# Kernel optimization log

Measured on AMD Instinct MI355X. Metric: run time of the kernel, lower is better.

The kernel has to match this reference:

```python
import jax, jax.numpy as jnp
import numpy as np

NN, D, H = 100000, 300, 1024   # nodes, embedding dim, hidden dim
NG, NS = 50000, 25000          # global vocab, sense vocab
B, T = 8, 128                  # batch, sequence length (state carried across all B*T steps)


def setup_inputs() -> dict:
    key = jax.random.key(0)
    ks = jax.random.split(key, 24)
    s = lambda i, shape: (jax.random.normal(ks[i], shape, jnp.float32) * 0.02)
    return {
        "x_idx": jax.random.randint(ks[0], (B, T), 0, NN),
        "X": jax.random.normal(ks[1], (NN, D), jnp.float32) * 0.1,
        "W_z_1": s(2, (D, H)), "U_z_1": s(3, (H, H)),
        "W_r_1": s(4, (D, H)), "U_r_1": s(5, (H, H)),
        "W_1": s(6, (D, H)), "b_W_1": jnp.zeros((H,), jnp.float32),
        "U_1": s(7, (H, H)), "b_U_1": jnp.zeros((H,), jnp.float32),
        "W_z_2": s(8, (H, H)), "U_z_2": s(9, (H, H)),
        "W_r_2": s(10, (H, H)), "U_r_2": s(11, (H, H)),
        "W_2": s(12, (H, H)), "b_W_2": jnp.zeros((H,), jnp.float32),
        "U_2": s(13, (H, H)), "b_U_2": jnp.zeros((H,), jnp.float32),
        "W_g": s(14, (H, NG)), "b_g": jnp.zeros((NG,), jnp.float32),
        "W_s": s(15, (H, NS)), "b_s": jnp.zeros((NS,), jnp.float32),
    }


def reference(x_idx, X, W_z_1, U_z_1, W_r_1, U_r_1, W_1, b_W_1, U_1, b_U_1,
              W_z_2, U_z_2, W_r_2, U_r_2, W_2, b_W_2, U_2, b_U_2,
              W_g, b_g, W_s, b_s):
    # The original loops over every sample of every sequence, carrying memory_h1/h2
    # across the whole batch; only X[x_indices[0]] feeds the GRU (the GAT-projected
    # neighbours are computed but never used). Dropout in eval mode = identity.
    idx = x_idx.reshape(-1)          # [S] flattened step order (seq-major per sample)
    emb = X[idx]                     # [S, D] currentword embeddings

    def step(carry, e):
        h1, h2 = carry
        z1 = jax.nn.sigmoid(e @ W_z_1 + h1 @ U_z_1)
        r1 = jax.nn.sigmoid(e @ W_r_1 + h1 @ U_r_1)
        ht1 = jnp.tanh((e @ W_1 + b_W_1) + ((r1 * h1) @ U_1 + b_U_1))
        h1n = z1 * ht1 + (1.0 - z1) * h1
        z2 = jax.nn.sigmoid(h1n @ W_z_2 + h2 @ U_z_2)
        r2 = jax.nn.sigmoid(h1n @ W_r_2 + h2 @ U_r_2)
        ht2 = jnp.tanh((h1n @ W_2 + b_W_2) + ((r2 * h2) @ U_2 + b_U_2))
        h2n = z2 * ht2 + (1.0 - z2) * h2
        return (h1n, h2n), h2n

    h0 = jnp.zeros((H,), emb.dtype)
    _, hs = jax.lax.scan(step, (h0, h0), emb)        # hs: [S, H]
    logp_g = jax.nn.log_softmax(hs @ W_g + b_g, axis=-1)   # [S, NG]
    logp_s = jax.nn.log_softmax(hs @ W_s + b_s, axis=-1)   # [S, NS]
    return logp_g, logp_s
```

## Files before the change

kernel.cpp:

```cpp
#include <hip/hip_runtime.h>

typedef __attribute__((ext_vector_type(4))) float f32x4;
typedef __attribute__((ext_vector_type(8))) __bf16 bf16x8;
typedef __attribute__((ext_vector_type(4))) unsigned short u16x4;

#define GPAD 40
#define KEEPF(x) asm volatile("" : "+v"(x))
#define PHYS(i) ((i) + (((i) >> 6) << 2))

__device__ unsigned long long g_h1s[1025 * 1024];
__device__ unsigned long long g_rh1[1024];
__device__ unsigned long long g_h2cur[1024];
__device__ unsigned long long g_rh2[1024];
__device__ float g_ExW[1024 * 3072];
__device__ float g_hs2[1024 * 1024];

__device__ __forceinline__ unsigned short f2bf(float x) {
  unsigned u = __builtin_bit_cast(unsigned, x);
  u += 0x7FFFu + ((u >> 16) & 1u);
  return (unsigned short)(u >> 16);
}
__device__ __forceinline__ unsigned long long packtv(unsigned tag, float v) {
  return ((unsigned long long)tag << 32) | (unsigned long long)__builtin_bit_cast(unsigned, v);
}
__device__ __forceinline__ unsigned long long aload(const unsigned long long* p) {
  return __hip_atomic_load(p, __ATOMIC_RELAXED, __HIP_MEMORY_SCOPE_AGENT);
}
__device__ __forceinline__ void astore(unsigned long long* p, unsigned long long v) {
  __hip_atomic_store(p, v, __ATOMIC_RELAXED, __HIP_MEMORY_SCOPE_AGENT);
}
__device__ __forceinline__ float lo32(unsigned long long v) {
  return __builtin_bit_cast(float, (unsigned)v);
}

__global__ void init_kernel() {
  int t = threadIdx.x;
  astore(&g_rh1[t], 0ull);
  astore(&g_h2cur[t], 0ull);
  astore(&g_rh2[t], 0ull);
}

__global__ __launch_bounds__(256, 1) void fused_scan(
    const float* __restrict__ ExW,
    const float* __restrict__ Uz1, const float* __restrict__ Ur1,
    const float* __restrict__ Uw1, const float* __restrict__ bU1,
    const float* __restrict__ Wz2, const float* __restrict__ Wr2,
    const float* __restrict__ Ww2,
    const float* __restrict__ Uz2, const float* __restrict__ Ur2,
    const float* __restrict__ Uw2,
    const float* __restrict__ bW2, const float* __restrict__ bU2,
    float* __restrict__ hs2)
{
  const int tid = threadIdx.x;
  const int c = tid & 15, q = tid >> 4;
  const int inw = tid & 63, wv = tid >> 6;
  __shared__ __align__(16) float h_s[1088];
  __shared__ __align__(16) float rh_s[1088];
  __shared__ __align__(16) float x_s[1088];
  __shared__ float pz[4][16], pr[4][16], pw[4][16];

  if (blockIdx.x < 64) {
    const int g = blockIdx.x;
    const int j = g * 16 + c;
    float uz[64], ur[64], uw[64];
#pragma unroll
    for (int i = 0; i < 64; ++i) uz[i] = Uz1[(size_t)(q * 64 + i) * 1024 + j];
#pragma unroll
    for (int i = 0; i < 64; ++i) ur[i] = Ur1[(size_t)(q * 64 + i) * 1024 + j];
#pragma unroll
    for (int i = 0; i < 64; ++i) uw[i] = Uw1[(size_t)(q * 64 + i) * 1024 + j];
#pragma unroll
    for (int i = 0; i < 64; ++i) { KEEPF(uz[i]); KEEPF(ur[i]); KEEPF(uw[i]); }
    const float bu = bU1[j];

    float zreg = 0.f, hold = 0.f;
    for (int s = 0; s < 1024; ++s) {
      float xz = 0.f, xr = 0.f, xw = 0.f;
      if (tid < 16) { xz = ExW[s * 3072 + j]; xw = ExW[s * 3072 + 2048 + j]; }
      else if (tid < 32) { xr = ExW[s * 3072 + 1024 + j]; }
      {
        const unsigned long long* sl = g_h1s + (size_t)s * 1024 + tid * 4;
        unsigned long long a0, a1, a2, a3;
        for (;;) {
          a0 = aload(sl); a1 = aload(sl + 1); a2 = aload(sl + 2); a3 = aload(sl + 3);
          unsigned bad = ((unsigned)(a0 >> 32) ^ (unsigned)s) | ((unsigned)(a1 >> 32) ^ (unsigned)s) |
                         ((unsigned)(a2 >> 32) ^ (unsigned)s) | ((unsigned)(a3 >> 32) ^ (unsigned)s);
          if (bad == 0u) break;
          __builtin_amdgcn_s_sleep(1);
        }
        f32x4 v; v.x = lo32(a0); v.y = lo32(a1); v.z = lo32(a2); v.w = lo32(a3);
        *(f32x4*)&h_s[PHYS(tid * 4)] = v;
      }
      __syncthreads();
      float az = 0.f, ar = 0.f;
      {
        const float* hp = h_s + q * 68;
#pragma unroll
        for (int i2 = 0; i2 < 16; ++i2) {
          f32x4 hv = *(const f32x4*)(hp + i2 * 4);
          az = fmaf(uz[i2 * 4 + 0], hv.x, az); az = fmaf(uz[i2 * 4 + 1], hv.y, az);
          az = fmaf(uz[i2 * 4 + 2], hv.z, az); az = fmaf(uz[i2 * 4 + 3], hv.w, az);
          ar = fmaf(ur[i2 * 4 + 0], hv.x, ar); ar = fmaf(ur[i2 * 4 + 1], hv.y, ar);
          ar = fmaf(ur[i2 * 4 + 2], hv.z, ar); ar = fmaf(ur[i2 * 4 + 3], hv.w, ar);
        }
      }
      az += __shfl_xor(az, 16, 64); az += __shfl_xor(az, 32, 64);
      ar += __shfl_xor(ar, 16, 64); ar += __shfl_xor(ar, 32, 64);
      if (inw < 16) { pz[wv][c] = az; pr[wv][c] = ar; }
      __syncthreads();
      if (tid < 32) {
        if (tid < 16) {
          float zz = pz[0][c] + pz[1][c] + pz[2][c] + pz[3][c] + xz;
          zreg = 1.f / (1.f + __expf(-zz));
          hold = h_s[PHYS(j)];
        } else {
          float rr = pr[0][c] + pr[1][c] + pr[2][c] + pr[3][c] + xr;
          float r = 1.f / (1.f + __expf(-rr));
          astore(&g_rh1[j], packtv((unsigned)(s + 1), r * h_s[PHYS(j)]));
        }
      }
      {
        const unsigned long long* sl = g_rh1 + tid * 4;
        unsigned long long a0, a1, a2, a3;
        const unsigned tg = (unsigned)(s + 1);
        for (;;) {
          a0 = aload(sl); a1 = aload(sl + 1); a2 = aload(sl + 2); a3 = aload(sl + 3);
          unsigned bad = ((unsigned)(a0 >> 32) ^ tg) | ((unsigned)(a1 >> 32) ^ tg) |
                         ((unsigned)(a2 >> 32) ^ tg) | ((unsigned)(a3 >> 32) ^ tg);
          if (bad == 0u) break;
          __builtin_amdgcn_s_sleep(1);
        }
        f32x4 v; v.x = lo32(a0); v.y = lo32(a1); v.z = lo32(a2); v.w = lo32(a3);
        *(f32x4*)&rh_s[PHYS(tid * 4)] = v;
      }
      __syncthreads();
      float aw = 0.f;
      {
        const float* rp = rh_s + q * 68;
#pragma unroll
        for (int i2 = 0; i2 < 16; ++i2) {
          f32x4 rv = *(const f32x4*)(rp + i2 * 4);
          aw = fmaf(uw[i2 * 4 + 0], rv.x, aw); aw = fmaf(uw[i2 * 4 + 1], rv.y, aw);
          aw = fmaf(uw[i2 * 4 + 2], rv.z, aw); aw = fmaf(uw[i2 * 4 + 3], rv.w, aw);
        }
      }
      aw += __shfl_xor(aw, 16, 64); aw += __shfl_xor(aw, 32, 64);
      if (inw < 16) pw[wv][c] = aw;
      __syncthreads();
      if (tid < 16) {
        float wwv = pw[0][c] + pw[1][c] + pw[2][c] + pw[3][c] + xw + bu;
        float ht = tanhf(wwv);
        float hn = zreg * ht + (1.f - zreg) * hold;
        astore(&g_h1s[(size_t)(s + 1) * 1024 + j], packtv((unsigned)(s + 1), hn));
      }
    }
  } else {
    const int g = blockIdx.x - 64;
    const int j = g * 16 + c;
    float uz[64], ur[64], uw[64], wz[64], wr[64], ww[64];
#pragma unroll
    for (int i = 0; i < 64; ++i) uz[i] = Uz2[(size_t)(q * 64 + i) * 1024 + j];
#pragma unroll
    for (int i = 0; i < 64; ++i) ur[i] = Ur2[(size_t)(q * 64 + i) * 1024 + j];
#pragma unroll
    for (int i = 0; i < 64; ++i) uw[i] = Uw2[(size_t)(q * 64 + i) * 1024 + j];
#pragma unroll
    for (int i = 0; i < 64; ++i) wz[i] = Wz2[(size_t)(q * 64 + i) * 1024 + j];
#pragma unroll
    for (int i = 0; i < 64; ++i) wr[i] = Wr2[(size_t)(q * 64 + i) * 1024 + j];
#pragma unroll
    for (int i = 0; i < 64; ++i) ww[i] = Ww2[(size_t)(q * 64 + i) * 1024 + j];
#pragma unroll
    for (int i = 0; i < 64; ++i) {
      KEEPF(uz[i]); KEEPF(ur[i]); KEEPF(uw[i]);
      KEEPF(wz[i]); KEEPF(wr[i]); KEEPF(ww[i]);
    }
    const float bu = bW2[j] + bU2[j];

    float zreg = 0.f, hold = 0.f;
    for (int s = 0; s < 1024; ++s) {
      {
        const unsigned long long* sh = g_h2cur + tid * 4;
        const unsigned long long* sx = g_h1s + (size_t)(s + 1) * 1024 + tid * 4;
        unsigned long long a0, a1, a2, a3, b0, b1, b2, b3;
        const unsigned tg = (unsigned)(s + 1);
        for (;;) {
          a0 = aload(sh); a1 = aload(sh + 1); a2 = aload(sh + 2); a3 = aload(sh + 3);
          b0 = aload(sx); b1 = aload(sx + 1); b2 = aload(sx + 2); b3 = aload(sx + 3);
          unsigned bad = ((unsigned)(a0 >> 32) ^ (unsigned)s) | ((unsigned)(a1 >> 32) ^ (unsigned)s) |
                         ((unsigned)(a2 >> 32) ^ (unsigned)s) | ((unsigned)(a3 >> 32) ^ (unsigned)s) |
                         ((unsigned)(b0 >> 32) ^ tg) | ((unsigned)(b1 >> 32) ^ tg) |
                         ((unsigned)(b2 >> 32) ^ tg) | ((unsigned)(b3 >> 32) ^ tg);
          if (bad == 0u) break;
          __builtin_amdgcn_s_sleep(1);
        }
        f32x4 v; v.x = lo32(a0); v.y = lo32(a1); v.z = lo32(a2); v.w = lo32(a3);
        *(f32x4*)&h_s[PHYS(tid * 4)] = v;
        f32x4 u4; u4.x = lo32(b0); u4.y = lo32(b1); u4.z = lo32(b2); u4.w = lo32(b3);
        *(f32x4*)&x_s[PHYS(tid * 4)] = u4;
      }
      __syncthreads();
      float az = 0.f, ar = 0.f;
      {
        const float* hp = h_s + q * 68;
        const float* xp = x_s + q * 68;
#pragma unroll
        for (int i2 = 0; i2 < 16; ++i2) {
          f32x4 hv = *(const f32x4*)(hp + i2 * 4);
          f32x4 xv = *(const f32x4*)(xp + i2 * 4);
          az = fmaf(uz[i2 * 4 + 0], hv.x, az); az = fmaf(uz[i2 * 4 + 1], hv.y, az);
          az = fmaf(uz[i2 * 4 + 2], hv.z, az); az = fmaf(uz[i2 * 4 + 3], hv.w, az);
          az = fmaf(wz[i2 * 4 + 0], xv.x, az); az = fmaf(wz[i2 * 4 + 1], xv.y, az);
          az = fmaf(wz[i2 * 4 + 2], xv.z, az); az = fmaf(wz[i2 * 4 + 3], xv.w, az);
          ar = fmaf(ur[i2 * 4 + 0], hv.x, ar); ar = fmaf(ur[i2 * 4 + 1], hv.y, ar);
          ar = fmaf(ur[i2 * 4 + 2], hv.z, ar); ar = fmaf(ur[i2 * 4 + 3], hv.w, ar);
          ar = fmaf(wr[i2 * 4 + 0], xv.x, ar); ar = fmaf(wr[i2 * 4 + 1], xv.y, ar);
          ar = fmaf(wr[i2 * 4 + 2], xv.z, ar); ar = fmaf(wr[i2 * 4 + 3], xv.w, ar);
        }
      }
      az += __shfl_xor(az, 16, 64); az += __shfl_xor(az, 32, 64);
      ar += __shfl_xor(ar, 16, 64); ar += __shfl_xor(ar, 32, 64);
      if (inw < 16) { pz[wv][c] = az; pr[wv][c] = ar; }
      __syncthreads();
      if (tid < 32) {
        if (tid < 16) {
          float zz = pz[0][c] + pz[1][c] + pz[2][c] + pz[3][c];
          zreg = 1.f / (1.f + __expf(-zz));
          hold = h_s[PHYS(j)];
        } else {
          float rr = pr[0][c] + pr[1][c] + pr[2][c] + pr[3][c];
          float r = 1.f / (1.f + __expf(-rr));
          astore(&g_rh2[j], packtv((unsigned)(s + 1), r * h_s[PHYS(j)]));
        }
      }
      {
        const unsigned long long* sl = g_rh2 + tid * 4;
        unsigned long long a0, a1, a2, a3;
        const unsigned tg = (unsigned)(s + 1);
        for (;;) {
          a0 = aload(sl); a1 = aload(sl + 1); a2 = aload(sl + 2); a3 = aload(sl + 3);
          unsigned bad = ((unsigned)(a0 >> 32) ^ tg) | ((unsigned)(a1 >> 32) ^ tg) |
                         ((unsigned)(a2 >> 32) ^ tg) | ((unsigned)(a3 >> 32) ^ tg);
          if (bad == 0u) break;
          __builtin_amdgcn_s_sleep(1);
        }
        f32x4 v; v.x = lo32(a0); v.y = lo32(a1); v.z = lo32(a2); v.w = lo32(a3);
        *(f32x4*)&rh_s[PHYS(tid * 4)] = v;
      }
      __syncthreads();
      float aw = 0.f;
      {
        const float* rp = rh_s + q * 68;
        const float* xp = x_s + q * 68;
#pragma unroll
        for (int i2 = 0; i2 < 16; ++i2) {
          f32x4 rv = *(const f32x4*)(rp + i2 * 4);
          f32x4 xv = *(const f32x4*)(xp + i2 * 4);
          aw = fmaf(uw[i2 * 4 + 0], rv.x, aw); aw = fmaf(uw[i2 * 4 + 1], rv.y, aw);
          aw = fmaf(uw[i2 * 4 + 2], rv.z, aw); aw = fmaf(uw[i2 * 4 + 3], rv.w, aw);
          aw = fmaf(ww[i2 * 4 + 0], xv.x, aw); aw = fmaf(ww[i2 * 4 + 1], xv.y, aw);
          aw = fmaf(ww[i2 * 4 + 2], xv.z, aw); aw = fmaf(ww[i2 * 4 + 3], xv.w, aw);
        }
      }
      aw += __shfl_xor(aw, 16, 64); aw += __shfl_xor(aw, 32, 64);
      if (inw < 16) pw[wv][c] = aw;
      __syncthreads();
      if (tid < 16) {
        float wwv = pw[0][c] + pw[1][c] + pw[2][c] + pw[3][c] + bu;
        float ht = tanhf(wwv);
        float hn = zreg * ht + (1.f - zreg) * hold;
        astore(&g_h2cur[j], packtv((unsigned)(s + 1), hn));
        hs2[(size_t)s * 1024 + j] = hn;
      }
    }
  }
}

__global__ __launch_bounds__(256, 1) void gemm_mfma(
    const float* __restrict__ A, const int* __restrict__ gidx, int lda,
    const float* __restrict__ B, int ldb,
    const float* __restrict__ bias,
    float* __restrict__ C, int ldc, int N, int K)
{
  __shared__ unsigned short As[128 * GPAD];
  __shared__ unsigned short Bs[128 * GPAD];
  const int tid = threadIdx.x;
  const int lane = tid & 63;
  const int wv = tid >> 6;
  const int wm = wv >> 1, wn = wv & 1;
  const int mbase = blockIdx.y * 128, nbase = blockIdx.x * 128;

  f32x4 acc[4][4];
#pragma unroll
  for (int i = 0; i < 4; ++i)
#pragma unroll
    for (int qq = 0; qq < 4; ++qq) acc[i][qq] = (f32x4){0.f, 0.f, 0.f, 0.f};

  const int ar = tid >> 1, ak = (tid & 1) * 16;
  const float* Arow;
  {
    int m = mbase + ar;
    long long gr = gidx ? (long long)gidx[m] : (long long)m;
    Arow = A + (size_t)gr * (size_t)lda;
  }
  const int bn = (tid >> 3) * 4;
  const int bk = (tid & 7) * 4;
  const bool nedge = (nbase + 128 > N);

  const int ksteps = (K + 31) >> 5;
  for (int ks = 0; ks < ksteps; ++ks) {
    const int k0 = ks << 5;
    __syncthreads();
    {
      float v[16];
      const int kg = k0 + ak;
      if (kg + 16 <= K) {
#pragma unroll
        for (int qq = 0; qq < 4; ++qq) {
          f32x4 t = *(const f32x4*)(Arow + kg + qq * 4);
          v[qq * 4 + 0] = t.x; v[qq * 4 + 1] = t.y; v[qq * 4 + 2] = t.z; v[qq * 4 + 3] = t.w;
        }
      } else {
#pragma unroll
        for (int i = 0; i < 16; ++i) v[i] = (kg + i < K) ? Arow[kg + i] : 0.f;
      }
#pragma unroll
      for (int qq = 0; qq < 4; ++qq) {
        u16x4 wq;
        wq.x = f2bf(v[qq * 4 + 0]); wq.y = f2bf(v[qq * 4 + 1]);
        wq.z = f2bf(v[qq * 4 + 2]); wq.w = f2bf(v[qq * 4 + 3]);
        *(u16x4*)&As[ar * GPAD + ak + qq * 4] = wq;
      }
    }
    {
      float bv[4][4];
#pragma unroll
      for (int kk = 0; kk < 4; ++kk) {
        int kglob = k0 + bk + kk;
        if (kglob < K) {
          if (!nedge) {
            f32x4 t = *(const f32x4*)(B + (size_t)kglob * (size_t)ldb + nbase + bn);
            bv[kk][0] = t.x; bv[kk][1] = t.y; bv[kk][2] = t.z; bv[kk][3] = t.w;
          } else {
#pragma unroll
            for (int nn = 0; nn < 4; ++nn) {
              int n = nbase + bn + nn;
              bv[kk][nn] = (n < N) ? B[(size_t)kglob * (size_t)ldb + n] : 0.f;
            }
          }
        } else {
          bv[kk][0] = bv[kk][1] = bv[kk][2] = bv[kk][3] = 0.f;
        }
      }
#pragma unroll
      for (int nn = 0; nn < 4; ++nn) {
        u16x4 wq;
        wq.x = f2bf(bv[0][nn]); wq.y = f2bf(bv[1][nn]);
        wq.z = f2bf(bv[2][nn]); wq.w = f2bf(bv[3][nn]);
        *(u16x4*)&Bs[(bn + nn) * GPAD + bk] = wq;
      }
    }
    __syncthreads();
    bf16x8 af[4], bfr[4];
    const int fr = lane & 15, fk = (lane >> 4) * 8;
#pragma unroll
    for (int mf = 0; mf < 4; ++mf)
      af[mf] = *(const bf16x8*)&As[(wm * 64 + mf * 16 + fr) * GPAD + fk];
#pragma unroll
    for (int nf = 0; nf < 4; ++nf)
      bfr[nf] = *(const bf16x8*)&Bs[(wn * 64 + nf * 16 + fr) * GPAD + fk];
#pragma unroll
    for (int mf = 0; mf < 4; ++mf)
#pragma unroll
      for (int nf = 0; nf < 4; ++nf)
        acc[mf][nf] = __builtin_amdgcn_mfma_f32_16x16x32_bf16(af[mf], bfr[nf], acc[mf][nf], 0, 0, 0);
  }
  const int fr = lane & 15, fq = lane >> 4;
#pragma unroll
  for (int nf = 0; nf < 4; ++nf) {
    int col = nbase + wn * 64 + nf * 16 + fr;
    if (col < N) {
      float bb = bias ? bias[col] : 0.f;
#pragma unroll
      for (int mf = 0; mf < 4; ++mf) {
        int row0 = mbase + wm * 64 + mf * 16 + fq * 4;
#pragma unroll
        for (int r = 0; r < 4; ++r)
          C[(size_t)(row0 + r) * (size_t)ldc + col] = acc[mf][nf][r] + bb;
      }
    }
  }
}

__global__ __launch_bounds__(256, 1) void logsoftmax_kernel(float* __restrict__ out) {
  const int row = blockIdx.x;
  float* p; int len;
  if (row < 1024) { p = out + (size_t)row * 50000u; len = 50000; }
  else            { p = out + 51200000ull + (size_t)(row - 1024) * 25000u; len = 25000; }
  const int tid = threadIdx.x;
  __shared__ float mred[4], sred[4];

  float m = -3.4e38f;
  for (int i = tid * 4; i < len; i += 1024) {
    f32x4 v = *(const f32x4*)(p + i);
    m = fmaxf(m, fmaxf(fmaxf(v.x, v.y), fmaxf(v.z, v.w)));
  }
#pragma unroll
  for (int off = 32; off >= 1; off >>= 1) m = fmaxf(m, __shfl_xor(m, off, 64));
  if ((tid & 63) == 0) mred[tid >> 6] = m;
  __syncthreads();
  m = fmaxf(fmaxf(mred[0], mred[1]), fmaxf(mred[2], mred[3]));

  float ssum = 0.f;
  for (int i = tid * 4; i < len; i += 1024) {
    f32x4 v = *(const f32x4*)(p + i);
    ssum += __expf(v.x - m) + __expf(v.y - m) + __expf(v.z - m) + __expf(v.w - m);
  }
#pragma unroll
  for (int off = 32; off >= 1; off >>= 1) ssum += __shfl_xor(ssum, off, 64);
  if ((tid & 63) == 0) sred[tid >> 6] = ssum;
  __syncthreads();
  const float lse = m + logf(sred[0] + sred[1] + sred[2] + sred[3]);

  for (int i = tid * 4; i < len; i += 1024) {
    f32x4 v = *(const f32x4*)(p + i);
    v.x -= lse; v.y -= lse; v.z -= lse; v.w -= lse;
    *(f32x4*)(p + i) = v;
  }
}

extern "C" void kernel_launch(void* const* d_in, const int* in_sizes, int n_in,
                              void* d_out, int out_size, void* d_ws, size_t ws_size,
                              hipStream_t stream) {
  (void)in_sizes; (void)n_in; (void)out_size; (void)d_ws; (void)ws_size;
  const int*   x_idx = (const int*)  d_in[0];
  const float* X     = (const float*)d_in[1];
  const float* W_z_1 = (const float*)d_in[2];
  const float* U_z_1 = (const float*)d_in[3];
  const float* W_r_1 = (const float*)d_in[4];
  const float* U_r_1 = (const float*)d_in[5];
  const float* W_1   = (const float*)d_in[6];
  const float* b_W_1 = (const float*)d_in[7];
  const float* U_1   = (const float*)d_in[8];
  const float* b_U_1 = (const float*)d_in[9];
  const float* W_z_2 = (const float*)d_in[10];
  const float* U_z_2 = (const float*)d_in[11];
  const float* W_r_2 = (const float*)d_in[12];
  const float* U_r_2 = (const float*)d_in[13];
  const float* W_2   = (const float*)d_in[14];
  const float* b_W_2 = (const float*)d_in[15];
  const float* U_2   = (const float*)d_in[16];
  const float* b_U_2 = (const float*)d_in[17];
  const float* W_g   = (const float*)d_in[18];
  const float* b_g   = (const float*)d_in[19];
  const float* W_s   = (const float*)d_in[20];
  const float* b_s   = (const float*)d_in[21];
  float* out = (float*)d_out;

  float *ExW, *hs2;
  unsigned long long* h1s;
  hipGetSymbolAddress((void**)&ExW, HIP_SYMBOL(g_ExW));
  hipGetSymbolAddress((void**)&hs2, HIP_SYMBOL(g_hs2));
  hipGetSymbolAddress((void**)&h1s, HIP_SYMBOL(g_h1s));

  const dim3 blk(256);

  init_kernel<<<dim3(1), dim3(1024), 0, stream>>>();
  hipMemsetAsync(h1s, 0, 1025ull * 1024 * sizeof(unsigned long long), stream);

  gemm_mfma<<<dim3(8, 8), blk, 0, stream>>>(X, x_idx, 300, W_z_1, 1024, nullptr, ExW + 0,    3072, 1024, 300);
  gemm_mfma<<<dim3(8, 8), blk, 0, stream>>>(X, x_idx, 300, W_r_1, 1024, nullptr, ExW + 1024, 3072, 1024, 300);
  gemm_mfma<<<dim3(8, 8), blk, 0, stream>>>(X, x_idx, 300, W_1,   1024, b_W_1,   ExW + 2048, 3072, 1024, 300);

  fused_scan<<<dim3(128), blk, 0, stream>>>(
      ExW, U_z_1, U_r_1, U_1, b_U_1,
      W_z_2, W_r_2, W_2, U_z_2, U_r_2, U_2, b_W_2, b_U_2, hs2);

  gemm_mfma<<<dim3(391, 8), blk, 0, stream>>>(hs2, nullptr, 1024, W_g, 50000, b_g, out,              50000, 50000, 1024);
  gemm_mfma<<<dim3(196, 8), blk, 0, stream>>>(hs2, nullptr, 1024, W_s, 25000, b_s, out + 51200000ll, 25000, 25000, 1024);
  logsoftmax_kernel<<<dim3(2048), blk, 0, stream>>>(out);
}
```

Before: 8.037 ms.

## Reduce GRU scan dots within a wavefront and split layer-2 over more blocks

```diff
diff --git a/kernel.cpp b/kernel.cpp
--- a/kernel.cpp
+++ b/kernel.cpp
@@ -52,16 +52,15 @@
     float* __restrict__ hs2)
 {
   const int tid = threadIdx.x;
-  const int c = tid & 15, q = tid >> 4;
-  const int inw = tid & 63, wv = tid >> 6;
+  const int wv = tid >> 6, inw = tid & 63;
   __shared__ __align__(16) float h_s[1088];
   __shared__ __align__(16) float rh_s[1088];
   __shared__ __align__(16) float x_s[1088];
-  __shared__ float pz[4][16], pr[4][16], pw[4][16];
 
   if (blockIdx.x < 64) {
     const int g = blockIdx.x;
-    const int j = g * 16 + c;
+    const int c2 = inw >> 4, q = inw & 15;
+    const int j = g * 16 + wv * 4 + c2;
     float uz[64], ur[64], uw[64];
 #pragma unroll
     for (int i = 0; i < 64; ++i) uz[i] = Uz1[(size_t)(q * 64 + i) * 1024 + j];
@@ -73,11 +72,11 @@
     for (int i = 0; i < 64; ++i) { KEEPF(uz[i]); KEEPF(ur[i]); KEEPF(uw[i]); }
     const float bu = bU1[j];
 
+    float xz = 0.f, xr = 0.f, xw = 0.f;
+    if (q == 0) { xz = ExW[j]; xr = ExW[1024 + j]; xw = ExW[2048 + j]; }
+
     float zreg = 0.f, hold = 0.f;
     for (int s = 0; s < 1024; ++s) {
-      float xz = 0.f, xr = 0.f, xw = 0.f;
-      if (tid < 16) { xz = ExW[s * 3072 + j]; xw = ExW[s * 3072 + 2048 + j]; }
-      else if (tid < 32) { xr = ExW[s * 3072 + 1024 + j]; }
       {
         const unsigned long long* sl = g_h1s + (size_t)s * 1024 + tid * 4;
         unsigned long long a0, a1, a2, a3;
@@ -92,32 +91,41 @@
         *(f32x4*)&h_s[PHYS(tid * 4)] = v;
       }
       __syncthreads();
-      float az = 0.f, ar = 0.f;
+      if (q == 0) hold = h_s[PHYS(j)];
+      float ar_ = 0.f;
       {
         const float* hp = h_s + q * 68;
 #pragma unroll
         for (int i2 = 0; i2 < 16; ++i2) {
           f32x4 hv = *(const f32x4*)(hp + i2 * 4);
-          az = fmaf(uz[i2 * 4 + 0], hv.x, az); az = fmaf(uz[i2 * 4 + 1], hv.y, az);
-          az = fmaf(uz[i2 * 4 + 2], hv.z, az); az = fmaf(uz[i2 * 4 + 3], hv.w, az);
-          ar = fmaf(ur[i2 * 4 + 0], hv.x, ar); ar = fmaf(ur[i2 * 4 + 1], hv.y, ar);
-          ar = fmaf(ur[i2 * 4 + 2], hv.z, ar); ar = fmaf(ur[i2 * 4 + 3], hv.w, ar);
-        }
-      }
-      az += __shfl_xor(az, 16, 64); az += __shfl_xor(az, 32, 64);
-      ar += __shfl_xor(ar, 16, 64); ar += __shfl_xor(ar, 32, 64);
-      if (inw < 16) { pz[wv][c] = az; pr[wv][c] = ar; }
-      __syncthreads();
-      if (tid < 32) {
-        if (tid < 16) {
-          float zz = pz[0][c] + pz[1][c] + pz[2][c] + pz[3][c] + xz;
-          zreg = 1.f / (1.f + __expf(-zz));
-          hold = h_s[PHYS(j)];
-        } else {
-          float rr = pr[0][c] + pr[1][c] + pr[2][c] + pr[3][c] + xr;
-          float r = 1.f / (1.f + __expf(-rr));
-          astore(&g_rh1[j], packtv((unsigned)(s + 1), r * h_s[PHYS(j)]));
-        }
+          ar_ = fmaf(ur[i2 * 4 + 0], hv.x, ar_); ar_ = fmaf(ur[i2 * 4 + 1], hv.y, ar_);
+          ar_ = fmaf(ur[i2 * 4 + 2], hv.z, ar_); ar_ = fmaf(ur[i2 * 4 + 3], hv.w, ar_);
+        }
+      }
+      ar_ += __shfl_xor(ar_, 1, 64); ar_ += __shfl_xor(ar_, 2, 64);
+      ar_ += __shfl_xor(ar_, 4, 64); ar_ += __shfl_xor(ar_, 8, 64);
+      if (q == 0) {
+        float r = 1.f / (1.f + __expf(-(ar_ + xr)));
+        astore(&g_rh1[j], packtv((unsigned)(s + 1), r * hold));
+      }
+      float az_ = 0.f;
+      {
+        const float* hp = h_s + q * 68;
+#pragma unroll
+        for (int i2 = 0; i2 < 16; ++i2) {
+          f32x4 hv = *(const f32x4*)(hp + i2 * 4);
+          az_ = fmaf(uz[i2 * 4 + 0], hv.x, az_); az_ = fmaf(uz[i2 * 4 + 1], hv.y, az_);
+          az_ = fmaf(uz[i2 * 4 + 2], hv.z, az_); az_ = fmaf(uz[i2 * 4 + 3], hv.w, az_);
+        }
+      }
+      az_ += __shfl_xor(az_, 1, 64); az_ += __shfl_xor(az_, 2, 64);
+      az_ += __shfl_xor(az_, 4, 64); az_ += __shfl_xor(az_, 8, 64);
+      if (q == 0) zreg = 1.f / (1.f + __expf(-(az_ + xz)));
+      float nxz = 0.f, nxr = 0.f, nxw = 0.f;
+      if (q == 0 && s < 1023) {
+        nxz = ExW[(s + 1) * 3072 + j];
+        nxr = ExW[(s + 1) * 3072 + 1024 + j];
+        nxw = ExW[(s + 1) * 3072 + 2048 + j];
       }
       {
         const unsigned long long* sl = g_rh1 + tid * 4;
@@ -134,44 +142,45 @@
         *(f32x4*)&rh_s[PHYS(tid * 4)] = v;
       }
       __syncthreads();
-      float aw = 0.f;
+      float aw_ = 0.f;
       {
         const float* rp = rh_s + q * 68;
 #pragma unroll
         for (int i2 = 0; i2 < 16; ++i2) {
           f32x4 rv = *(const f32x4*)(rp + i2 * 4);
-          aw = fmaf(uw[i2 * 4 + 0], rv.x, aw); aw = fmaf(uw[i2 * 4 + 1], rv.y, aw);
-          aw = fmaf(uw[i2 * 4 + 2], rv.z, aw); aw = fmaf(uw[i2 * 4 + 3], rv.w, aw);
-        }
-      }
-      aw += __shfl_xor(aw, 16, 64); aw += __shfl_xor(aw, 32, 64);
-      if (inw < 16) pw[wv][c] = aw;
-      __syncthreads();
-      if (tid < 16) {
-        float wwv = pw[0][c] + pw[1][c] + pw[2][c] + pw[3][c] + xw + bu;
-        float ht = tanhf(wwv);
+          aw_ = fmaf(uw[i2 * 4 + 0], rv.x, aw_); aw_ = fmaf(uw[i2 * 4 + 1], rv.y, aw_);
+          aw_ = fmaf(uw[i2 * 4 + 2], rv.z, aw_); aw_ = fmaf(uw[i2 * 4 + 3], rv.w, aw_);
+        }
+      }
+      aw_ += __shfl_xor(aw_, 1, 64); aw_ += __shfl_xor(aw_, 2, 64);
+      aw_ += __shfl_xor(aw_, 4, 64); aw_ += __shfl_xor(aw_, 8, 64);
+      if (q == 0) {
+        float ht = tanhf(aw_ + xw + bu);
         float hn = zreg * ht + (1.f - zreg) * hold;
         astore(&g_h1s[(size_t)(s + 1) * 1024 + j], packtv((unsigned)(s + 1), hn));
       }
+      xz = nxz; xr = nxr; xw = nxw;
     }
   } else {
     const int g = blockIdx.x - 64;
-    const int j = g * 16 + c;
-    float uz[64], ur[64], uw[64], wz[64], wr[64], ww[64];
-#pragma unroll
-    for (int i = 0; i < 64; ++i) uz[i] = Uz2[(size_t)(q * 64 + i) * 1024 + j];
-#pragma unroll
-    for (int i = 0; i < 64; ++i) ur[i] = Ur2[(size_t)(q * 64 + i) * 1024 + j];
-#pragma unroll
-    for (int i = 0; i < 64; ++i) uw[i] = Uw2[(size_t)(q * 64 + i) * 1024 + j];
-#pragma unroll
-    for (int i = 0; i < 64; ++i) wz[i] = Wz2[(size_t)(q * 64 + i) * 1024 + j];
-#pragma unroll
-    for (int i = 0; i < 64; ++i) wr[i] = Wr2[(size_t)(q * 64 + i) * 1024 + j];
-#pragma unroll
-    for (int i = 0; i < 64; ++i) ww[i] = Ww2[(size_t)(q * 64 + i) * 1024 + j];
-#pragma unroll
-    for (int i = 0; i < 64; ++i) {
+    const int c2 = inw >> 5, q = inw & 31;
+    const int j = g * 8 + wv * 2 + c2;
+    const int sb = q * 32 + ((q >> 1) << 2);
+    float uz[32], ur[32], uw[32], wz[32], wr[32], ww[32];
+#pragma unroll
+    for (int i = 0; i < 32; ++i) uz[i] = Uz2[(size_t)(q * 32 + i) * 1024 + j];
+#pragma unroll
+    for (int i = 0; i < 32; ++i) ur[i] = Ur2[(size_t)(q * 32 + i) * 1024 + j];
+#pragma unroll
+    for (int i = 0; i < 32; ++i) uw[i] = Uw2[(size_t)(q * 32 + i) * 1024 + j];
+#pragma unroll
+    for (int i = 0; i < 32; ++i) wz[i] = Wz2[(size_t)(q * 32 + i) * 1024 + j];
+#pragma unroll
+    for (int i = 0; i < 32; ++i) wr[i] = Wr2[(size_t)(q * 32 + i) * 1024 + j];
+#pragma unroll
+    for (int i = 0; i < 32; ++i) ww[i] = Ww2[(size_t)(q * 32 + i) * 1024 + j];
+#pragma unroll
+    for (int i = 0; i < 32; ++i) {
       KEEPF(uz[i]); KEEPF(ur[i]); KEEPF(uw[i]);
       KEEPF(wz[i]); KEEPF(wr[i]); KEEPF(ww[i]);
     }
@@ -200,39 +209,46 @@
         *(f32x4*)&x_s[PHYS(tid * 4)] = u4;
       }
       __syncthreads();
-      float az = 0.f, ar = 0.f;
-      {
-        const float* hp = h_s + q * 68;
-        const float* xp = x_s + q * 68;
-#pragma unroll
-        for (int i2 = 0; i2 < 16; ++i2) {
+      if (q == 0) hold = h_s[PHYS(j)];
+      float ar_ = 0.f;
+      {
+        const float* hp = h_s + sb;
+        const float* xp = x_s + sb;
+#pragma unroll
+        for (int i2 = 0; i2 < 8; ++i2) {
           f32x4 hv = *(const f32x4*)(hp + i2 * 4);
           f32x4 xv = *(const f32x4*)(xp + i2 * 4);
-          az = fmaf(uz[i2 * 4 + 0], hv.x, az); az = fmaf(uz[i2 * 4 + 1], hv.y, az);
-          az = fmaf(uz[i2 * 4 + 2], hv.z, az); az = fmaf(uz[i2 * 4 + 3], hv.w, az);
-          az = fmaf(wz[i2 * 4 + 0], xv.x, az); az = fmaf(wz[i2 * 4 + 1], xv.y, az);
-          az = fmaf(wz[i2 * 4 + 2], xv.z, az); az = fmaf(wz[i2 * 4 + 3], xv.w, az);
-          ar = fmaf(ur[i2 * 4 + 0], hv.x, ar); ar = fmaf(ur[i2 * 4 + 1], hv.y, ar);
-          ar = fmaf(ur[i2 * 4 + 2], hv.z, ar); ar = fmaf(ur[i2 * 4 + 3], hv.w, ar);
-          ar = fmaf(wr[i2 * 4 + 0], xv.x, ar); ar = fmaf(wr[i2 * 4 + 1], xv.y, ar);
-          ar = fmaf(wr[i2 * 4 + 2], xv.z, ar); ar = fmaf(wr[i2 * 4 + 3], xv.w, ar);
-        }
-      }
-      az += __shfl_xor(az, 16, 64); az += __shfl_xor(az, 32, 64);
-      ar += __shfl_xor(ar, 16, 64); ar += __shfl_xor(ar, 32, 64);
-      if (inw < 16) { pz[wv][c] = az; pr[wv][c] = ar; }
-      __syncthreads();
-      if (tid < 32) {
-        if (tid < 16) {
-          float zz = pz[0][c] + pz[1][c] + pz[2][c] + pz[3][c];
-          zreg = 1.f / (1.f + __expf(-zz));
-          hold = h_s[PHYS(j)];
-        } else {
-          float rr = pr[0][c] + pr[1][c] + pr[2][c] + pr[3][c];
-          float r = 1.f / (1.f + __expf(-rr));
-          astore(&g_rh2[j], packtv((unsigned)(s + 1), r * h_s[PHYS(j)]));
-        }
-      }
+          ar_ = fmaf(ur[i2 * 4 + 0], hv.x, ar_); ar_ = fmaf(ur[i2 * 4 + 1], hv.y, ar_);
+          ar_ = fmaf(ur[i2 * 4 + 2], hv.z, ar_); ar_ = fmaf(ur[i2 * 4 + 3], hv.w, ar_);
+          ar_ = fmaf(wr[i2 * 4 + 0], xv.x, ar_); ar_ = fmaf(wr[i2 * 4 + 1], xv.y, ar_);
+          ar_ = fmaf(wr[i2 * 4 + 2], xv.z, ar_); ar_ = fmaf(wr[i2 * 4 + 3], xv.w, ar_);
+        }
+      }
+      ar_ += __shfl_xor(ar_, 1, 64); ar_ += __shfl_xor(ar_, 2, 64);
+      ar_ += __shfl_xor(ar_, 4, 64); ar_ += __shfl_xor(ar_, 8, 64);
+      ar_ += __shfl_xor(ar_, 16, 64);
+      if (q == 0) {
+        float r = 1.f / (1.f + __expf(-ar_));
+        astore(&g_rh2[j], packtv((unsigned)(s + 1), r * hold));
+      }
+      float az_ = 0.f;
+      {
+        const float* hp = h_s + sb;
+        const float* xp = x_s + sb;
+#pragma unroll
+        for (int i2 = 0; i2 < 8; ++i2) {
+          f32x4 hv = *(const f32x4*)(hp + i2 * 4);
+          f32x4 xv = *(const f32x4*)(xp + i2 * 4);
+          az_ = fmaf(uz[i2 * 4 + 0], hv.x, az_); az_ = fmaf(uz[i2 * 4 + 1], hv.y, az_);
+          az_ = fmaf(uz[i2 * 4 + 2], hv.z, az_); az_ = fmaf(uz[i2 * 4 + 3], hv.w, az_);
+          az_ = fmaf(wz[i2 * 4 + 0], xv.x, az_); az_ = fmaf(wz[i2 * 4 + 1], xv.y, az_);
+          az_ = fmaf(wz[i2 * 4 + 2], xv.z, az_); az_ = fmaf(wz[i2 * 4 + 3], xv.w, az_);
+        }
+      }
+      az_ += __shfl_xor(az_, 1, 64); az_ += __shfl_xor(az_, 2, 64);
+      az_ += __shfl_xor(az_, 4, 64); az_ += __shfl_xor(az_, 8, 64);
+      az_ += __shfl_xor(az_, 16, 64);
+      if (q == 0) zreg = 1.f / (1.f + __expf(-az_));
       {
         const unsigned long long* sl = g_rh2 + tid * 4;
         unsigned long long a0, a1, a2, a3;
@@ -248,26 +264,25 @@
         *(f32x4*)&rh_s[PHYS(tid * 4)] = v;
       }
       __syncthreads();
-      float aw = 0.f;
-      {
-        const float* rp = rh_s + q * 68;
-        const float* xp = x_s + q * 68;
-#pragma unroll
-        for (int i2 = 0; i2 < 16; ++i2) {
+      float aw_ = 0.f;
+      {
+        const float* rp = rh_s + sb;
+        const float* xp = x_s + sb;
+#pragma unroll
+        for (int i2 = 0; i2 < 8; ++i2) {
           f32x4 rv = *(const f32x4*)(rp + i2 * 4);
           f32x4 xv = *(const f32x4*)(xp + i2 * 4);
-          aw = fmaf(uw[i2 * 4 + 0], rv.x, aw); aw = fmaf(uw[i2 * 4 + 1], rv.y, aw);
-          aw = fmaf(uw[i2 * 4 + 2], rv.z, aw); aw = fmaf(uw[i2 * 4 + 3], rv.w, aw);
-          aw = fmaf(ww[i2 * 4 + 0], xv.x, aw); aw = fmaf(ww[i2 * 4 + 1], xv.y, aw);
-          aw = fmaf(ww[i2 * 4 + 2], xv.z, aw); aw = fmaf(ww[i2 * 4 + 3], xv.w, aw);
-        }
-      }
-      aw += __shfl_xor(aw, 16, 64); aw += __shfl_xor(aw, 32, 64);
-      if (inw < 16) pw[wv][c] = aw;
-      __syncthreads();
-      if (tid < 16) {
-        float wwv = pw[0][c] + pw[1][c] + pw[2][c] + pw[3][c] + bu;
-        float ht = tanhf(wwv);
+          aw_ = fmaf(uw[i2 * 4 + 0], rv.x, aw_); aw_ = fmaf(uw[i2 * 4 + 1], rv.y, aw_);
+          aw_ = fmaf(uw[i2 * 4 + 2], rv.z, aw_); aw_ = fmaf(uw[i2 * 4 + 3], rv.w, aw_);
+          aw_ = fmaf(ww[i2 * 4 + 0], xv.x, aw_); aw_ = fmaf(ww[i2 * 4 + 1], xv.y, aw_);
+          aw_ = fmaf(ww[i2 * 4 + 2], xv.z, aw_); aw_ = fmaf(ww[i2 * 4 + 3], xv.w, aw_);
+        }
+      }
+      aw_ += __shfl_xor(aw_, 1, 64); aw_ += __shfl_xor(aw_, 2, 64);
+      aw_ += __shfl_xor(aw_, 4, 64); aw_ += __shfl_xor(aw_, 8, 64);
+      aw_ += __shfl_xor(aw_, 16, 64);
+      if (q == 0) {
+        float ht = tanhf(aw_ + bu);
         float hn = zreg * ht + (1.f - zreg) * hold;
         astore(&g_h2cur[j], packtv((unsigned)(s + 1), hn));
         hs2[(size_t)s * 1024 + j] = hn;
@@ -472,7 +487,7 @@
   gemm_mfma<<<dim3(8, 8), blk, 0, stream>>>(X, x_idx, 300, W_r_1, 1024, nullptr, ExW + 1024, 3072, 1024, 300);
   gemm_mfma<<<dim3(8, 8), blk, 0, stream>>>(X, x_idx, 300, W_1,   1024, b_W_1,   ExW + 2048, 3072, 1024, 300);
 
-  fused_scan<<<dim3(128), blk, 0, stream>>>(
+  fused_scan<<<dim3(192), blk, 0, stream>>>(
       ExW, U_z_1, U_r_1, U_1, b_U_1,
       W_z_2, W_r_2, W_2, U_z_2, U_r_2, U_2, b_W_2, b_U_2, hs2);
 
```

Result: faster. 6.803 ms (-15.4%).
